# Kernel tuning notes

Hardware: AMD Instinct MI355X
Metric: run time of the kernel (lower is better)

The kernel has to match this reference:

```python
import jax, jax.numpy as jnp
import numpy as np

N, E = 50000, 800000
D_IN, HID, H, C, E_DIM = 128, 128, 4, 32, 32  # C = HID // H


def setup_inputs() -> dict:
    key = jax.random.key(0)
    ks = jax.random.split(key, 16)
    def lin(k, fan_in, fan_out):
        return jax.random.normal(k, (fan_in, fan_out), jnp.float32) / np.sqrt(fan_in)
    return {
        "x": jax.random.normal(ks[0], (N, D_IN), jnp.float32),
        "edge_index": jax.random.randint(ks[1], (2, E), 0, N, jnp.int32),
        "edge_attr": jax.random.normal(ks[2], (E, E_DIM), jnp.float32),
        # TransformerConv params (bias=True on q/k/v and skip; lin_edge has no bias in PyG)
        "Wq": lin(ks[3], D_IN, HID), "bq": jnp.zeros((HID,), jnp.float32),
        "Wk": lin(ks[4], D_IN, HID), "bk": jnp.zeros((HID,), jnp.float32),
        "Wv": lin(ks[5], D_IN, HID), "bv": jnp.zeros((HID,), jnp.float32),
        "We": lin(ks[6], E_DIM, HID),
        "Wskip": lin(ks[7], D_IN, HID), "bskip": jnp.zeros((HID,), jnp.float32),
        # MLP([HID, HID, HID]) -> two Linear layers, GELU(tanh) after each (plain_last=False)
        "W1": lin(ks[8], HID, HID), "b1": jnp.zeros((HID,), jnp.float32),
        "W2": lin(ks[9], HID, HID), "b2": jnp.zeros((HID,), jnp.float32),
    }


def reference(x, edge_index, edge_attr, Wq, bq, Wk, bk, Wv, bv, We, Wskip, bskip, W1, b1, W2, b2):
    src, dst = edge_index[0], edge_index[1]  # messages flow src(j) -> dst(i)
    n = x.shape[0]
    q = (x @ Wq + bq).reshape(n, H, C)
    k = (x @ Wk + bk).reshape(n, H, C)
    v = (x @ Wv + bv).reshape(n, H, C)
    e = (edge_attr @ We).reshape(-1, H, C)          # [E,H,C]
    kj = k[src] + e                                  # gather + edge lift
    vj = v[src] + e
    alpha = jnp.einsum("ehc,ehc->eh", q[dst], kj) / np.sqrt(C)  # [E,H]
    # segment softmax over destination neighborhoods (PyG softmax semantics)
    amax = jax.ops.segment_max(alpha, dst, num_segments=n)      # [N,H]
    amax = jnp.where(jnp.isfinite(amax), amax, 0.0)
    ex = jnp.exp(alpha - amax[dst])
    denom = jax.ops.segment_sum(ex, dst, num_segments=n)
    alpha = ex / (denom[dst] + 1e-16)
    # (attention dropout p=0.3 is inactive in eval mode)
    agg = jax.ops.segment_sum(vj * alpha[:, :, None], dst, num_segments=n)  # [N,H,C]
    out = agg.reshape(n, HID) + (x @ Wskip + bskip)  # concat heads + root skip
    # residual MLP: gelu(tanh) after every layer since plain_last=False, norm=None
    h = jax.nn.gelu(out @ W1 + b1, approximate=True)
    h = jax.nn.gelu(h @ W2 + b2, approximate=True)
    return out + h
```

## Files before the change

### kernel.cpp

```cpp
#include <hip/hip_runtime.h>
#include <math.h>


#define D 128
#define EDIM 32

using bf16x8 = __attribute__((ext_vector_type(8))) short;
using f32x4  = __attribute__((ext_vector_type(4))) float;
using ushort8 = __attribute__((ext_vector_type(8))) unsigned short;

__device__ inline unsigned short f2bf(float f) {
    unsigned int u = __float_as_uint(f);
    u += 0x7FFFu + ((u >> 16) & 1u);
    return (unsigned short)(u >> 16);
}
__device__ inline float bf2f(unsigned short h) {
    return __uint_as_float(((unsigned int)h) << 16);
}
__device__ inline float gelu_fast(float x) {
    float x3 = x * x * x;
    float u = 0.7978845608028654f * (x + 0.044715f * x3);
    float t = 1.f - 2.f / (__expf(2.f * u) + 1.f);
    return 0.5f * x * (1.f + t);
}
__device__ inline float quad_add(float x) {
    int a = __builtin_amdgcn_update_dpp(0, __float_as_int(x), 0xB1, 0xF, 0xF, true);
    x += __int_as_float(a);
    a = __builtin_amdgcn_update_dpp(0, __float_as_int(x), 0x4E, 0xF, 0xF, true);
    x += __int_as_float(a);
    return x;
}

__device__ inline bf16x8 ldsB(const unsigned short* sw, int col, int kk0) {
    return *(const bf16x8*)(sw + col * 128 + (kk0 ^ ((col & 7) << 3)));
}

__global__ __launch_bounds__(256) void prep_wt(
    const float* __restrict__ Wq, const float* __restrict__ Wk,
    const float* __restrict__ Wv, const float* __restrict__ Wsk,
    const float* __restrict__ W1, const float* __restrict__ W2,
    const float* __restrict__ We, const float* __restrict__ bq,
    unsigned short* __restrict__ Wt, float* __restrict__ bqE)
{
    int t = blockIdx.x * 256 + threadIdx.x;
    int m = t >> 14;
    int r = t & 16383;
    if (m >= 8) {
        if (r < 128) {
            const int hb = r & 96, k = r & 31;
            const float* wek = We + (size_t)k * D + hb;
            float s = 0.f;
#pragma unroll 8
            for (int c = 0; c < 32; ++c) s = fmaf(bq[hb + c], wek[c], s);
            bqE[r] = s;
        }
        return;
    }
    int col = r & 127, kk = r >> 7;
    float v;
    if (m < 6) {
        const float* W = (m == 0) ? Wq : (m == 1) ? Wk : (m == 2) ? Wv
                       : (m == 3) ? Wsk : (m == 4) ? W1 : W2;
        v = W[(size_t)kk * D + col];
    } else if (m == 6) {
        const int hb = col & 96;
        const float* wqr = Wq + (size_t)kk * D + hb;
        const float* wer = We + (size_t)(col & 31) * D + hb;
        float s = 0.f;
#pragma unroll 8
        for (int c = 0; c < 32; ++c) s = fmaf(wqr[c], wer[c], s);
        v = s;
    } else {
        v = ((kk >> 5) == (col >> 5)) ? We[(size_t)(kk & 31) * D + col] : 0.f;
    }
    Wt[(size_t)m * 16384 + (size_t)col * 128 + (kk ^ ((col & 7) << 3))] = f2bf(v);
}

__global__ __launch_bounds__(256) void gemm_qkvs(
    const float* __restrict__ x, const unsigned short* __restrict__ Wt,
    const float* __restrict__ bq, const float* __restrict__ bk,
    const float* __restrict__ bv, const float* __restrict__ bs,
    const float* __restrict__ bqE,
    unsigned short* __restrict__ QA, unsigned short* __restrict__ KV,
    float* __restrict__ S, int N)
{
    __shared__ unsigned short sw[16384];
    const int m = blockIdx.y;
    const int widx = (m < 4) ? m : 6;
    const int t = threadIdx.x;
    const int lane = t & 63;
    const int w = t >> 6;
    const int row0 = blockIdx.x * 64 + w * 16;
    const int lrow = lane & 15;
    const int kb = (lane >> 4) * 8;
    const int rq = (lane >> 4) * 4;

    const unsigned short* gsrc = Wt + (size_t)widx * 16384;
    ushort8 stg[8];
#pragma unroll
    for (int it = 0; it < 8; ++it)
        stg[it] = *(const ushort8*)(gsrc + (t + it * 256) * 8);

    bf16x8 af[4];
    {
        int ar = row0 + lrow; if (ar > N - 1) ar = N - 1;
        const float* xr = x + (size_t)ar * D + kb;
#pragma unroll
        for (int kf = 0; kf < 4; ++kf) {
            float4 p0 = *(const float4*)(xr + kf * 32);
            float4 p1 = *(const float4*)(xr + kf * 32 + 4);
            bf16x8 a;
            a[0] = (short)f2bf(p0.x); a[1] = (short)f2bf(p0.y);
            a[2] = (short)f2bf(p0.z); a[3] = (short)f2bf(p0.w);
            a[4] = (short)f2bf(p1.x); a[5] = (short)f2bf(p1.y);
            a[6] = (short)f2bf(p1.z); a[7] = (short)f2bf(p1.w);
            af[kf] = a;
        }
    }

#pragma unroll
    for (int it = 0; it < 8; ++it)
        *(ushort8*)(&sw[(t + it * 256) * 8]) = stg[it];
    __syncthreads();

    const float* bias = (m == 0) ? bq : (m == 1) ? bk : (m == 2) ? bv
                      : (m == 3) ? bs : bqE;
    f32x4 acc[8];
#pragma unroll
    for (int nf = 0; nf < 8; ++nf) acc[nf] = (f32x4){0.f, 0.f, 0.f, 0.f};
#pragma unroll
    for (int nf = 0; nf < 8; ++nf) {
        const int col = nf * 16 + lrow;
#pragma unroll
        for (int kf = 0; kf < 4; ++kf)
            acc[nf] = __builtin_amdgcn_mfma_f32_16x16x32_bf16(
                af[kf], ldsB(sw, col, kf * 32 + kb), acc[nf], 0, 0, 0);
    }
#pragma unroll
    for (int nf = 0; nf < 8; ++nf) {
        const int col = nf * 16 + lrow;
        const float bb = bias[col];
#pragma unroll
        for (int i = 0; i < 4; ++i) {
            int r = row0 + rq + i;
            if (r < N) {
                float v = acc[nf][i] + bb;
                if (m == 0)      QA[(size_t)r * 256 + col]       = f2bf(v);
                else if (m == 1) KV[(size_t)r * 256 + col]       = f2bf(v);
                else if (m == 2) KV[(size_t)r * 256 + 128 + col] = f2bf(v);
                else if (m == 3) S[(size_t)r * D + col]          = v;
                else             QA[(size_t)r * 256 + 128 + col] = f2bf(v);
            }
        }
    }
}

__global__ __launch_bounds__(256) void hist_kernel(
    const int* __restrict__ EI, int* __restrict__ deg, int E)
{
    int e = blockIdx.x * 256 + threadIdx.x;
    if (e < E) atomicAdd(&deg[EI[E + e]], 1);
}

__global__ __launch_bounds__(1024) void scanA(
    const int* __restrict__ deg, int* __restrict__ rowptr,
    int* __restrict__ psums, int N)
{
    __shared__ int tmp[1024];
    const int t = threadIdx.x;
    const int i = blockIdx.x * 1024 + t;
    int v = (i < N) ? deg[i] : 0;
    tmp[t] = v;
    __syncthreads();
    for (int off = 1; off < 1024; off <<= 1) {
        int add = (t >= off) ? tmp[t - off] : 0;
        __syncthreads();
        tmp[t] += add;
        __syncthreads();
    }
    if (i < N) rowptr[i + 1] = tmp[t];
    if (t == 1023) psums[blockIdx.x] = tmp[1023];
}

__global__ __launch_bounds__(1024) void scanB(int* __restrict__ psums, int nb)
{
    __shared__ int tmp[1024];
    const int t = threadIdx.x;
    int v = (t < nb) ? psums[t] : 0;
    tmp[t] = v;
    __syncthreads();
    for (int off = 1; off < 1024; off <<= 1) {
        int add = (t >= off) ? tmp[t - off] : 0;
        __syncthreads();
        tmp[t] += add;
        __syncthreads();
    }
    if (t < nb) psums[t] = tmp[t] - v;
}

__global__ __launch_bounds__(256) void scanC(
    int* __restrict__ rowptr, int* __restrict__ cursor,
    const int* __restrict__ psums, int N)
{
    int i = blockIdx.x * 256 + threadIdx.x;
    if (i == 0) { rowptr[0] = 0; cursor[0] = 0; }
    if (i < N) {
        int val = rowptr[i + 1] + psums[i >> 10];
        rowptr[i + 1] = val;
        if (i + 1 < N) cursor[i + 1] = val;
    }
}

__global__ __launch_bounds__(256) void scatter_kernel(
    const int* __restrict__ EI, const float* __restrict__ EA,
    int* __restrict__ cursor, int* __restrict__ srcs,
    unsigned short* __restrict__ EAP, int E)
{
    int e = blockIdx.x * 256 + threadIdx.x;
    if (e >= E) return;
    int dst = EI[E + e];
    int pos = atomicAdd(&cursor[dst], 1);
    srcs[pos] = EI[e];
    const float4* s4 = (const float4*)(EA + (size_t)e * EDIM);
    unsigned short* op = EAP + (size_t)pos * EDIM;
#pragma unroll
    for (int j = 0; j < 4; ++j) {
        float4 a = s4[2 * j], b = s4[2 * j + 1];
        ushort8 u;
        u[0] = f2bf(a.x); u[1] = f2bf(a.y); u[2] = f2bf(a.z); u[3] = f2bf(a.w);
        u[4] = f2bf(b.x); u[5] = f2bf(b.y); u[6] = f2bf(b.z); u[7] = f2bf(b.w);
        *(ushort8*)(op + j * 8) = u;
    }
}

__global__ __launch_bounds__(256) void gather_pass(
    const int* __restrict__ rowptr, const int* __restrict__ srcs,
    const unsigned short* __restrict__ EAP,
    const unsigned short* __restrict__ QA, const unsigned short* __restrict__ KV,
    float* __restrict__ SB, unsigned short* __restrict__ SAS, int N)
{
    const int lane = threadIdx.x & 63;
    const int wid = threadIdx.x >> 6;
    const int n = blockIdx.x * 4 + wid;
    if (n >= N) return;
    const int g = lane & 15;
    const int grp = lane >> 4;
    const int eoff = (g & 3) * 8;

    float q8[8], qe8[8];
    {
        const unsigned short* qa = QA + (size_t)n * 256 + g * 8;
        bf16x8 qb  = *(const bf16x8*)(qa);
        bf16x8 qeb = *(const bf16x8*)(qa + 128);
#pragma unroll
        for (int j = 0; j < 8; ++j) {
            q8[j]  = bf2f((unsigned short)qb[j]);
            qe8[j] = bf2f((unsigned short)qeb[j]);
        }
    }

    float acc[8], sa[8], den = 0.f;
#pragma unroll
    for (int j = 0; j < 8; ++j) { acc[j] = 0.f; sa[j] = 0.f; }

    const int i0 = rowptr[n], i1 = rowptr[n + 1];

    int iA = i0 + grp, iB = iA + 4;
    int sA = (iA < i1) ? srcs[iA] : -1;
    int sB = (iB < i1) ? srcs[iB] : -1;

    for (int b = i0; b < i1; b += 8) {
        const int iA2 = iA + 8, iB2 = iB + 8;
        const int sA2 = (iA2 < i1) ? srcs[iA2] : -1;
        const int sB2 = (iB2 < i1) ? srcs[iB2] : -1;

        bf16x8 kA = {0,0,0,0,0,0,0,0}, vA = kA, eA = kA;
        bf16x8 kB = kA, vB = kA, eB = kA;
        if (sA >= 0) {
            const unsigned short* kv = KV + (size_t)sA * 256 + g * 8;
            kA = *(const bf16x8*)(kv);
            vA = *(const bf16x8*)(kv + 128);
            eA = *(const bf16x8*)(EAP + (size_t)iA * EDIM + eoff);
        }
        if (sB >= 0) {
            const unsigned short* kv = KV + (size_t)sB * 256 + g * 8;
            kB = *(const bf16x8*)(kv);
            vB = *(const bf16x8*)(kv + 128);
            eB = *(const bf16x8*)(EAP + (size_t)iB * EDIM + eoff);
        }

        {
            float ef[8];
            float p = 0.f;
#pragma unroll
            for (int j = 0; j < 8; ++j) {
                ef[j] = bf2f((unsigned short)eA[j]);
                p = fmaf(q8[j], bf2f((unsigned short)kA[j]),
                         fmaf(ef[j], qe8[j], p));
            }
            p = quad_add(p);
            const float ex = (sA >= 0) ? __expf(p * 0.17677669529663689f) : 0.f;
            den += ex;
#pragma unroll
            for (int j = 0; j < 8; ++j) {
                acc[j] = fmaf(ex, bf2f((unsigned short)vA[j]), acc[j]);
                sa[j]  = fmaf(ex, ef[j], sa[j]);
            }
        }
        {
            float ef[8];
            float p = 0.f;
#pragma unroll
            for (int j = 0; j < 8; ++j) {
                ef[j] = bf2f((unsigned short)eB[j]);
                p = fmaf(q8[j], bf2f((unsigned short)kB[j]),
                         fmaf(ef[j], qe8[j], p));
            }
            p = quad_add(p);
            const float ex = (sB >= 0) ? __expf(p * 0.17677669529663689f) : 0.f;
            den += ex;
#pragma unroll
            for (int j = 0; j < 8; ++j) {
                acc[j] = fmaf(ex, bf2f((unsigned short)vB[j]), acc[j]);
                sa[j]  = fmaf(ex, ef[j], sa[j]);
            }
        }
        iA = iA2; iB = iB2; sA = sA2; sB = sB2;
    }

#pragma unroll
    for (int off = 16; off <= 32; off <<= 1) {
        den += __shfl_xor(den, off, 64);
#pragma unroll
        for (int j = 0; j < 8; ++j) {
            acc[j] += __shfl_xor(acc[j], off, 64);
            sa[j]  += __shfl_xor(sa[j],  off, 64);
        }
    }

    if (grp == 0) {
        const float rden = 1.f / (den + 1e-16f);
        float* so = SB + (size_t)n * D + g * 8;
        unsigned short* po = SAS + (size_t)n * D + g * 8;
#pragma unroll
        for (int j = 0; j < 8; ++j) {
            so[j] = fmaf(acc[j], rden, so[j]);
            po[j] = f2bf(sa[j] * rden);
        }
    }
}

__global__ __launch_bounds__(256) void combine_mlp1(
    float* __restrict__ SB, const unsigned short* __restrict__ SAS,
    const unsigned short* __restrict__ WtC, const unsigned short* __restrict__ Wt1,
    const float* __restrict__ b1, unsigned short* __restrict__ H1, int N)
{
    __shared__ unsigned short sw[16384];
    __shared__ unsigned short bounce[64 * 136];
    const int t = threadIdx.x;
    const int lane = t & 63;
    const int w = t >> 6;
    const int row0 = blockIdx.x * 64 + w * 16;
    const int lrow = lane & 15;
    const int kb = (lane >> 4) * 8;
    const int rq = (lane >> 4) * 4;

    ushort8 stg[8];
#pragma unroll
    for (int it = 0; it < 8; ++it)
        stg[it] = *(const ushort8*)(WtC + (t + it * 256) * 8);

    bf16x8 af[4];
    {
        int ar = row0 + lrow; if (ar > N - 1) ar = N - 1;
        const unsigned short* xr = SAS + (size_t)ar * D + kb;
#pragma unroll
        for (int kf = 0; kf < 4; ++kf) af[kf] = *(const bf16x8*)(xr + kf * 32);
    }
    f32x4 acc[8];
#pragma unroll
    for (int nf = 0; nf < 8; ++nf) {
        const int col = nf * 16 + lrow;
#pragma unroll
        for (int i = 0; i < 4; ++i) {
            int r = row0 + rq + i;
            acc[nf][i] = (r < N) ? SB[(size_t)r * D + col] : 0.f;
        }
    }

#pragma unroll
    for (int it = 0; it < 8; ++it)
        *(ushort8*)(&sw[(t + it * 256) * 8]) = stg[it];
    __syncthreads();

#pragma unroll
    for (int nf = 0; nf < 8; ++nf) {
        const int col = nf * 16 + lrow;
#pragma unroll
        for (int kf = 0; kf < 4; ++kf)
            acc[nf] = __builtin_amdgcn_mfma_f32_16x16x32_bf16(
                af[kf], ldsB(sw, col, kf * 32 + kb), acc[nf], 0, 0, 0);
    }
    __syncthreads();

#pragma unroll
    for (int it = 0; it < 8; ++it)
        stg[it] = *(const ushort8*)(Wt1 + (t + it * 256) * 8);
#pragma unroll
    for (int nf = 0; nf < 8; ++nf) {
        const int col = nf * 16 + lrow;
#pragma unroll
        for (int i = 0; i < 4; ++i) {
            int r = row0 + rq + i;
            float v = acc[nf][i];
            bounce[(w * 16 + rq + i) * 136 + col] = f2bf(v);
            if (r < N) SB[(size_t)r * D + col] = v;
        }
    }
#pragma unroll
    for (int it = 0; it < 8; ++it)
        *(ushort8*)(&sw[(t + it * 256) * 8]) = stg[it];
    __syncthreads();

    bf16x8 af2[4];
#pragma unroll
    for (int kf = 0; kf < 4; ++kf)
        af2[kf] = *(const bf16x8*)(&bounce[(w * 16 + lrow) * 136 + kb + kf * 32]);
    f32x4 acc2[8];
#pragma unroll
    for (int nf = 0; nf < 8; ++nf) acc2[nf] = (f32x4){0.f, 0.f, 0.f, 0.f};
#pragma unroll
    for (int nf = 0; nf < 8; ++nf) {
        const int col = nf * 16 + lrow;
#pragma unroll
        for (int kf = 0; kf < 4; ++kf)
            acc2[nf] = __builtin_amdgcn_mfma_f32_16x16x32_bf16(
                af2[kf], ldsB(sw, col, kf * 32 + kb), acc2[nf], 0, 0, 0);
    }
#pragma unroll
    for (int nf = 0; nf < 8; ++nf) {
        const int col = nf * 16 + lrow;
        const float bb = b1[col];
#pragma unroll
        for (int i = 0; i < 4; ++i) {
            int r = row0 + rq + i;
            if (r < N) H1[(size_t)r * D + col] = f2bf(gelu_fast(acc2[nf][i] + bb));
        }
    }
}

__global__ __launch_bounds__(256) void mlp2_kernel(
    const unsigned short* __restrict__ H1, const float* __restrict__ OUT,
    const unsigned short* __restrict__ Wt2, const float* __restrict__ b2,
    float* __restrict__ FINAL, int N)
{
    __shared__ unsigned short sw[16384];
    const int t = threadIdx.x;
    const int lane = t & 63;
    const int w = t >> 6;
    const int row0 = blockIdx.x * 64 + w * 16;
    const int lrow = lane & 15;
    const int kb = (lane >> 4) * 8;
    const int rq = (lane >> 4) * 4;

    ushort8 stg[8];
#pragma unroll
    for (int it = 0; it < 8; ++it)
        stg[it] = *(const ushort8*)(Wt2 + (t + it * 256) * 8);

    bf16x8 af[4];
    {
        int ar = row0 + lrow; if (ar > N - 1) ar = N - 1;
        const unsigned short* xr = H1 + (size_t)ar * D + kb;
#pragma unroll
        for (int kf = 0; kf < 4; ++kf) af[kf] = *(const bf16x8*)(xr + kf * 32);
    }

#pragma unroll
    for (int it = 0; it < 8; ++it)
        *(ushort8*)(&sw[(t + it * 256) * 8]) = stg[it];
    __syncthreads();

    f32x4 acc[8];
#pragma unroll
    for (int nf = 0; nf < 8; ++nf) acc[nf] = (f32x4){0.f, 0.f, 0.f, 0.f};
#pragma unroll
    for (int nf = 0; nf < 8; ++nf) {
        const int col = nf * 16 + lrow;
#pragma unroll
        for (int kf = 0; kf < 4; ++kf)
            acc[nf] = __builtin_amdgcn_mfma_f32_16x16x32_bf16(
                af[kf], ldsB(sw, col, kf * 32 + kb), acc[nf], 0, 0, 0);
    }
#pragma unroll
    for (int nf = 0; nf < 8; ++nf) {
        const int col = nf * 16 + lrow;
        const float bb = b2[col];
#pragma unroll
        for (int i = 0; i < 4; ++i) {
            int r = row0 + rq + i;
            if (r < N) {
                size_t o = (size_t)r * D + col;
                FINAL[o] = OUT[o] + gelu_fast(acc[nf][i] + bb);
            }
        }
    }
}

extern "C" void kernel_launch(void* const* d_in, const int* in_sizes, int n_in,
                              void* d_out, int out_size, void* d_ws, size_t ws_size,
                              hipStream_t stream)
{
    const float* x   = (const float*)d_in[0];
    const int*   EI  = (const int*)  d_in[1];
    const float* EA  = (const float*)d_in[2];
    const float* Wq  = (const float*)d_in[3];
    const float* bq  = (const float*)d_in[4];
    const float* Wk  = (const float*)d_in[5];
    const float* bk  = (const float*)d_in[6];
    const float* Wv  = (const float*)d_in[7];
    const float* bv  = (const float*)d_in[8];
    const float* We  = (const float*)d_in[9];
    const float* Wsk = (const float*)d_in[10];
    const float* bsk = (const float*)d_in[11];
    const float* W1  = (const float*)d_in[12];
    const float* b1  = (const float*)d_in[13];
    const float* W2  = (const float*)d_in[14];
    const float* b2  = (const float*)d_in[15];

    const int N = in_sizes[0] / D;
    const int E = in_sizes[1] / 2;

    char* p = (char*)d_ws;
    auto alloc = [&](size_t bytes) -> void* {
        void* r = (void*)p;
        p += (bytes + 255) & ~(size_t)255;
        return r;
    };
    float*          Sb     = (float*)         alloc((size_t)N * D * 4);
    unsigned short* QAb    = (unsigned short*)alloc((size_t)N * 256 * 2);
    unsigned short* KVb    = (unsigned short*)alloc((size_t)N * 256 * 2);
    unsigned short* SASb   = (unsigned short*)alloc((size_t)N * D * 2);
    unsigned short* EAPb   = (unsigned short*)alloc((size_t)E * EDIM * 2);
    int*            srcsb  = (int*)           alloc((size_t)E * 4);
    unsigned short* Wt     = (unsigned short*)alloc((size_t)8 * 16384 * 2);
    float*          bqEb   = (float*)         alloc((size_t)128 * 4);
    int*            deg    = (int*)           alloc((size_t)N * 4);
    int*            rowptr = (int*)           alloc((size_t)(N + 1) * 4);
    int*            cursor = (int*)           alloc((size_t)(N + 1) * 4);
    int*            psums  = (int*)           alloc((size_t)1024 * 4);

    unsigned short* H1b = QAb;

    hipMemsetAsync(deg, 0, (size_t)N * sizeof(int), stream);

    const int NB = (N + 63) / 64;
    const int EB = (E + 255) / 256;
    const int SB_ = (N + 1023) / 1024;

    prep_wt<<<513, 256, 0, stream>>>(Wq, Wk, Wv, Wsk, W1, W2, We, bq, Wt, bqEb);

    gemm_qkvs<<<dim3(NB, 5), 256, 0, stream>>>(x, Wt, bq, bk, bv, bsk, bqEb,
                                               QAb, KVb, Sb, N);

    hist_kernel<<<EB, 256, 0, stream>>>(EI, deg, E);
    scanA<<<SB_, 1024, 0, stream>>>(deg, rowptr, psums, N);
    scanB<<<1, 1024, 0, stream>>>(psums, SB_);
    scanC<<<(N + 255) / 256, 256, 0, stream>>>(rowptr, cursor, psums, N);
    scatter_kernel<<<EB, 256, 0, stream>>>(EI, EA, cursor, srcsb, EAPb, E);

    gather_pass<<<(N + 3) / 4, 256, 0, stream>>>(
        rowptr, srcsb, EAPb, QAb, KVb, Sb, SASb, N);

    combine_mlp1<<<NB, 256, 0, stream>>>(Sb, SASb, Wt + (size_t)7 * 16384,
                                         Wt + (size_t)4 * 16384, b1, H1b, N);
    mlp2_kernel<<<NB, 256, 0, stream>>>(H1b, Sb, Wt + (size_t)5 * 16384, b2,
                                        (float*)d_out, N);
}
```

Before: 299.2 us.

## Merge prep with histogram, scatter with QKV GEMM, and fuse both MLP layers

The weight-prep kernel now also runs the degree histogram in extra blocks, and the CSR scatter runs in the same launch as the QKV/skip GEMM through a flat block index. The two MLP kernels become one: the combined output stays in registers, and the first MLP activation goes through LDS instead of a global H1 buffer. This removes several launches, the H1 write and read, and the re-read of the output in the second MLP. In exchange, the fused MLP kernel uses more registers and LDS, and the mixed-role launches give heterogeneous blocks that may balance poorly.

```diff
diff --git a/kernel.cpp b/kernel.cpp
--- a/kernel.cpp
+++ b/kernel.cpp
@@ -35,13 +35,19 @@
     return *(const bf16x8*)(sw + col * 128 + (kk0 ^ ((col & 7) << 3)));
 }
 
-__global__ __launch_bounds__(256) void prep_wt(
+__global__ __launch_bounds__(256) void prep_wt_hist(
     const float* __restrict__ Wq, const float* __restrict__ Wk,
     const float* __restrict__ Wv, const float* __restrict__ Wsk,
     const float* __restrict__ W1, const float* __restrict__ W2,
     const float* __restrict__ We, const float* __restrict__ bq,
-    unsigned short* __restrict__ Wt, float* __restrict__ bqE)
-{
+    unsigned short* __restrict__ Wt, float* __restrict__ bqE,
+    const int* __restrict__ EI, int* __restrict__ deg, int E)
+{
+    if (blockIdx.x >= 513) {
+        int e = (blockIdx.x - 513) * 256 + threadIdx.x;
+        if (e < E) atomicAdd(&deg[EI[E + e]], 1);
+        return;
+    }
     int t = blockIdx.x * 256 + threadIdx.x;
     int m = t >> 14;
     int r = t & 16383;
@@ -76,21 +82,95 @@
     Wt[(size_t)m * 16384 + (size_t)col * 128 + (kk ^ ((col & 7) << 3))] = f2bf(v);
 }
 
-__global__ __launch_bounds__(256) void gemm_qkvs(
+__global__ __launch_bounds__(1024) void scanA(
+    const int* __restrict__ deg, int* __restrict__ rowptr,
+    int* __restrict__ psums, int N)
+{
+    __shared__ int tmp[1024];
+    const int t = threadIdx.x;
+    const int i = blockIdx.x * 1024 + t;
+    int v = (i < N) ? deg[i] : 0;
+    tmp[t] = v;
+    __syncthreads();
+    for (int off = 1; off < 1024; off <<= 1) {
+        int add = (t >= off) ? tmp[t - off] : 0;
+        __syncthreads();
+        tmp[t] += add;
+        __syncthreads();
+    }
+    if (i < N) rowptr[i + 1] = tmp[t];
+    if (t == 1023) psums[blockIdx.x] = tmp[1023];
+}
+
+__global__ __launch_bounds__(1024) void scanB(int* __restrict__ psums, int nb)
+{
+    __shared__ int tmp[1024];
+    const int t = threadIdx.x;
+    int v = (t < nb) ? psums[t] : 0;
+    tmp[t] = v;
+    __syncthreads();
+    for (int off = 1; off < 1024; off <<= 1) {
+        int add = (t >= off) ? tmp[t - off] : 0;
+        __syncthreads();
+        tmp[t] += add;
+        __syncthreads();
+    }
+    if (t < nb) psums[t] = tmp[t] - v;
+}
+
+__global__ __launch_bounds__(256) void scanC(
+    int* __restrict__ rowptr, int* __restrict__ cursor,
+    const int* __restrict__ psums, int N)
+{
+    int i = blockIdx.x * 256 + threadIdx.x;
+    if (i == 0) { rowptr[0] = 0; cursor[0] = 0; }
+    if (i < N) {
+        int val = rowptr[i + 1] + psums[i >> 10];
+        rowptr[i + 1] = val;
+        if (i + 1 < N) cursor[i + 1] = val;
+    }
+}
+
+__global__ __launch_bounds__(256) void mega_scatter_gemm(
+    const int* __restrict__ EI, const float* __restrict__ EA,
+    int* __restrict__ cursor, int* __restrict__ srcs,
+    unsigned short* __restrict__ EAP, int E, int EB,
     const float* __restrict__ x, const unsigned short* __restrict__ Wt,
     const float* __restrict__ bq, const float* __restrict__ bk,
     const float* __restrict__ bv, const float* __restrict__ bs,
     const float* __restrict__ bqE,
     unsigned short* __restrict__ QA, unsigned short* __restrict__ KV,
-    float* __restrict__ S, int N)
+    float* __restrict__ S, int N, int NB)
 {
     __shared__ unsigned short sw[16384];
-    const int m = blockIdx.y;
+    const int t = threadIdx.x;
+
+    if ((int)blockIdx.x < EB) {
+        int e = blockIdx.x * 256 + t;
+        if (e >= E) return;
+        int dst = EI[E + e];
+        int pos = atomicAdd(&cursor[dst], 1);
+        srcs[pos] = EI[e];
+        const float4* s4 = (const float4*)(EA + (size_t)e * EDIM);
+        unsigned short* op = EAP + (size_t)pos * EDIM;
+#pragma unroll
+        for (int j = 0; j < 4; ++j) {
+            float4 a = s4[2 * j], b = s4[2 * j + 1];
+            ushort8 u;
+            u[0] = f2bf(a.x); u[1] = f2bf(a.y); u[2] = f2bf(a.z); u[3] = f2bf(a.w);
+            u[4] = f2bf(b.x); u[5] = f2bf(b.y); u[6] = f2bf(b.z); u[7] = f2bf(b.w);
+            *(ushort8*)(op + j * 8) = u;
+        }
+        return;
+    }
+
+    const int bid = blockIdx.x - EB;
+    const int m = bid / NB;
+    const int bx = bid - m * NB;
     const int widx = (m < 4) ? m : 6;
-    const int t = threadIdx.x;
     const int lane = t & 63;
     const int w = t >> 6;
-    const int row0 = blockIdx.x * 64 + w * 16;
+    const int row0 = bx * 64 + w * 16;
     const int lrow = lane & 15;
     const int kb = (lane >> 4) * 8;
     const int rq = (lane >> 4) * 4;
@@ -155,84 +235,6 @@
     }
 }
 
-__global__ __launch_bounds__(256) void hist_kernel(
-    const int* __restrict__ EI, int* __restrict__ deg, int E)
-{
-    int e = blockIdx.x * 256 + threadIdx.x;
-    if (e < E) atomicAdd(&deg[EI[E + e]], 1);
-}
-
-__global__ __launch_bounds__(1024) void scanA(
-    const int* __restrict__ deg, int* __restrict__ rowptr,
-    int* __restrict__ psums, int N)
-{
-    __shared__ int tmp[1024];
-    const int t = threadIdx.x;
-    const int i = blockIdx.x * 1024 + t;
-    int v = (i < N) ? deg[i] : 0;
-    tmp[t] = v;
-    __syncthreads();
-    for (int off = 1; off < 1024; off <<= 1) {
-        int add = (t >= off) ? tmp[t - off] : 0;
-        __syncthreads();
-        tmp[t] += add;
-        __syncthreads();
-    }
-    if (i < N) rowptr[i + 1] = tmp[t];
-    if (t == 1023) psums[blockIdx.x] = tmp[1023];
-}
-
-__global__ __launch_bounds__(1024) void scanB(int* __restrict__ psums, int nb)
-{
-    __shared__ int tmp[1024];
-    const int t = threadIdx.x;
-    int v = (t < nb) ? psums[t] : 0;
-    tmp[t] = v;
-    __syncthreads();
-    for (int off = 1; off < 1024; off <<= 1) {
-        int add = (t >= off) ? tmp[t - off] : 0;
-        __syncthreads();
-        tmp[t] += add;
-        __syncthreads();
-    }
-    if (t < nb) psums[t] = tmp[t] - v;
-}
-
-__global__ __launch_bounds__(256) void scanC(
-    int* __restrict__ rowptr, int* __restrict__ cursor,
-    const int* __restrict__ psums, int N)
-{
-    int i = blockIdx.x * 256 + threadIdx.x;
-    if (i == 0) { rowptr[0] = 0; cursor[0] = 0; }
-    if (i < N) {
-        int val = rowptr[i + 1] + psums[i >> 10];
-        rowptr[i + 1] = val;
-        if (i + 1 < N) cursor[i + 1] = val;
-    }
-}
-
-__global__ __launch_bounds__(256) void scatter_kernel(
-    const int* __restrict__ EI, const float* __restrict__ EA,
-    int* __restrict__ cursor, int* __restrict__ srcs,
-    unsigned short* __restrict__ EAP, int E)
-{
-    int e = blockIdx.x * 256 + threadIdx.x;
-    if (e >= E) return;
-    int dst = EI[E + e];
-    int pos = atomicAdd(&cursor[dst], 1);
-    srcs[pos] = EI[e];
-    const float4* s4 = (const float4*)(EA + (size_t)e * EDIM);
-    unsigned short* op = EAP + (size_t)pos * EDIM;
-#pragma unroll
-    for (int j = 0; j < 4; ++j) {
-        float4 a = s4[2 * j], b = s4[2 * j + 1];
-        ushort8 u;
-        u[0] = f2bf(a.x); u[1] = f2bf(a.y); u[2] = f2bf(a.z); u[3] = f2bf(a.w);
-        u[4] = f2bf(b.x); u[5] = f2bf(b.y); u[6] = f2bf(b.z); u[7] = f2bf(b.w);
-        *(ushort8*)(op + j * 8) = u;
-    }
-}
-
 __global__ __launch_bounds__(256) void gather_pass(
     const int* __restrict__ rowptr, const int* __restrict__ srcs,
     const unsigned short* __restrict__ EAP,
@@ -350,10 +352,12 @@
     }
 }
 
-__global__ __launch_bounds__(256) void combine_mlp1(
-    float* __restrict__ SB, const unsigned short* __restrict__ SAS,
+__global__ __launch_bounds__(256) void fused_mlp(
+    const float* __restrict__ SB, const unsigned short* __restrict__ SAS,
     const unsigned short* __restrict__ WtC, const unsigned short* __restrict__ Wt1,
-    const float* __restrict__ b1, unsigned short* __restrict__ H1, int N)
+    const unsigned short* __restrict__ Wt2,
+    const float* __restrict__ b1, const float* __restrict__ b2,
+    float* __restrict__ FINAL, int N)
 {
     __shared__ unsigned short sw[16384];
     __shared__ unsigned short bounce[64 * 136];
@@ -377,17 +381,16 @@
 #pragma unroll
         for (int kf = 0; kf < 4; ++kf) af[kf] = *(const bf16x8*)(xr + kf * 32);
     }
-    f32x4 acc[8];
+    f32x4 out[8];
 #pragma unroll
     for (int nf = 0; nf < 8; ++nf) {
         const int col = nf * 16 + lrow;
 #pragma unroll
         for (int i = 0; i < 4; ++i) {
             int r = row0 + rq + i;
-            acc[nf][i] = (r < N) ? SB[(size_t)r * D + col] : 0.f;
-        }
-    }
-
+            out[nf][i] = (r < N) ? SB[(size_t)r * D + col] : 0.f;
+        }
+    }
 #pragma unroll
     for (int it = 0; it < 8; ++it)
         *(ushort8*)(&sw[(t + it * 256) * 8]) = stg[it];
@@ -398,8 +401,8 @@
         const int col = nf * 16 + lrow;
 #pragma unroll
         for (int kf = 0; kf < 4; ++kf)
-            acc[nf] = __builtin_amdgcn_mfma_f32_16x16x32_bf16(
-                af[kf], ldsB(sw, col, kf * 32 + kb), acc[nf], 0, 0, 0);
+            out[nf] = __builtin_amdgcn_mfma_f32_16x16x32_bf16(
+                af[kf], ldsB(sw, col, kf * 32 + kb), out[nf], 0, 0, 0);
     }
     __syncthreads();
 
@@ -410,12 +413,8 @@
     for (int nf = 0; nf < 8; ++nf) {
         const int col = nf * 16 + lrow;
 #pragma unroll
-        for (int i = 0; i < 4; ++i) {
-            int r = row0 + rq + i;
-            float v = acc[nf][i];
-            bounce[(w * 16 + rq + i) * 136 + col] = f2bf(v);
-            if (r < N) SB[(size_t)r * D + col] = v;
-        }
+        for (int i = 0; i < 4; ++i)
+            bounce[(w * 16 + rq + i) * 136 + col] = f2bf(out[nf][i]);
     }
 #pragma unroll
     for (int it = 0; it < 8; ++it)
@@ -437,72 +436,48 @@
             acc2[nf] = __builtin_amdgcn_mfma_f32_16x16x32_bf16(
                 af2[kf], ldsB(sw, col, kf * 32 + kb), acc2[nf], 0, 0, 0);
     }
+    __syncthreads();
+
+#pragma unroll
+    for (int it = 0; it < 8; ++it)
+        stg[it] = *(const ushort8*)(Wt2 + (t + it * 256) * 8);
 #pragma unroll
     for (int nf = 0; nf < 8; ++nf) {
         const int col = nf * 16 + lrow;
         const float bb = b1[col];
+#pragma unroll
+        for (int i = 0; i < 4; ++i)
+            bounce[(w * 16 + rq + i) * 136 + col] = f2bf(gelu_fast(acc2[nf][i] + bb));
+    }
+#pragma unroll
+    for (int it = 0; it < 8; ++it)
+        *(ushort8*)(&sw[(t + it * 256) * 8]) = stg[it];
+    __syncthreads();
+
+    bf16x8 af3[4];
+#pragma unroll
+    for (int kf = 0; kf < 4; ++kf)
+        af3[kf] = *(const bf16x8*)(&bounce[(w * 16 + lrow) * 136 + kb + kf * 32]);
+    f32x4 acc3[8];
+#pragma unroll
+    for (int nf = 0; nf < 8; ++nf) acc3[nf] = (f32x4){0.f, 0.f, 0.f, 0.f};
+#pragma unroll
+    for (int nf = 0; nf < 8; ++nf) {
+        const int col = nf * 16 + lrow;
+#pragma unroll
+        for (int kf = 0; kf < 4; ++kf)
+            acc3[nf] = __builtin_amdgcn_mfma_f32_16x16x32_bf16(
+                af3[kf], ldsB(sw, col, kf * 32 + kb), acc3[nf], 0, 0, 0);
+    }
+#pragma unroll
+    for (int nf = 0; nf < 8; ++nf) {
+        const int col = nf * 16 + lrow;
+        const float bb = b2[col];
 #pragma unroll
         for (int i = 0; i < 4; ++i) {
             int r = row0 + rq + i;
-            if (r < N) H1[(size_t)r * D + col] = f2bf(gelu_fast(acc2[nf][i] + bb));
-        }
-    }
-}
-
-__global__ __launch_bounds__(256) void mlp2_kernel(
-    const unsigned short* __restrict__ H1, const float* __restrict__ OUT,
-    const unsigned short* __restrict__ Wt2, const float* __restrict__ b2,
-    float* __restrict__ FINAL, int N)
-{
-    __shared__ unsigned short sw[16384];
-    const int t = threadIdx.x;
-    const int lane = t & 63;
-    const int w = t >> 6;
-    const int row0 = blockIdx.x * 64 + w * 16;
-    const int lrow = lane & 15;
-    const int kb = (lane >> 4) * 8;
-    const int rq = (lane >> 4) * 4;
-
-    ushort8 stg[8];
-#pragma unroll
-    for (int it = 0; it < 8; ++it)
-        stg[it] = *(const ushort8*)(Wt2 + (t + it * 256) * 8);
-
-    bf16x8 af[4];
-    {
-        int ar = row0 + lrow; if (ar > N - 1) ar = N - 1;
-        const unsigned short* xr = H1 + (size_t)ar * D + kb;
-#pragma unroll
-        for (int kf = 0; kf < 4; ++kf) af[kf] = *(const bf16x8*)(xr + kf * 32);
-    }
-
-#pragma unroll
-    for (int it = 0; it < 8; ++it)
-        *(ushort8*)(&sw[(t + it * 256) * 8]) = stg[it];
-    __syncthreads();
-
-    f32x4 acc[8];
-#pragma unroll
-    for (int nf = 0; nf < 8; ++nf) acc[nf] = (f32x4){0.f, 0.f, 0.f, 0.f};
-#pragma unroll
-    for (int nf = 0; nf < 8; ++nf) {
-        const int col = nf * 16 + lrow;
-#pragma unroll
-        for (int kf = 0; kf < 4; ++kf)
-            acc[nf] = __builtin_amdgcn_mfma_f32_16x16x32_bf16(
-                af[kf], ldsB(sw, col, kf * 32 + kb), acc[nf], 0, 0, 0);
-    }
-#pragma unroll
-    for (int nf = 0; nf < 8; ++nf) {
-        const int col = nf * 16 + lrow;
-        const float bb = b2[col];
-#pragma unroll
-        for (int i = 0; i < 4; ++i) {
-            int r = row0 + rq + i;
-            if (r < N) {
-                size_t o = (size_t)r * D + col;
-                FINAL[o] = OUT[o] + gelu_fast(acc[nf][i] + bb);
-            }
+            if (r < N)
+                FINAL[(size_t)r * D + col] = out[nf][i] + gelu_fast(acc3[nf][i] + bb);
         }
     }
 }
@@ -550,30 +525,29 @@
     int*            cursor = (int*)           alloc((size_t)(N + 1) * 4);
     int*            psums  = (int*)           alloc((size_t)1024 * 4);
 
-    unsigned short* H1b = QAb;
-
     hipMemsetAsync(deg, 0, (size_t)N * sizeof(int), stream);
 
     const int NB = (N + 63) / 64;
     const int EB = (E + 255) / 256;
     const int SB_ = (N + 1023) / 1024;
 
-    prep_wt<<<513, 256, 0, stream>>>(Wq, Wk, Wv, Wsk, W1, W2, We, bq, Wt, bqEb);
-
-    gemm_qkvs<<<dim3(NB, 5), 256, 0, stream>>>(x, Wt, bq, bk, bv, bsk, bqEb,
-                                               QAb, KVb, Sb, N);
-
-    hist_kernel<<<EB, 256, 0, stream>>>(EI, deg, E);
+    prep_wt_hist<<<513 + EB, 256, 0, stream>>>(Wq, Wk, Wv, Wsk, W1, W2, We, bq,
+                                               Wt, bqEb, EI, deg, E);
+
     scanA<<<SB_, 1024, 0, stream>>>(deg, rowptr, psums, N);
     scanB<<<1, 1024, 0, stream>>>(psums, SB_);
     scanC<<<(N + 255) / 256, 256, 0, stream>>>(rowptr, cursor, psums, N);
-    scatter_kernel<<<EB, 256, 0, stream>>>(EI, EA, cursor, srcsb, EAPb, E);
+
+    mega_scatter_gemm<<<EB + 5 * NB, 256, 0, stream>>>(
+        EI, EA, cursor, srcsb, EAPb, E, EB,
+        x, Wt, bq, bk, bv, bsk, bqEb, QAb, KVb, Sb, N, NB);
 
     gather_pass<<<(N + 3) / 4, 256, 0, stream>>>(
         rowptr, srcsb, EAPb, QAb, KVb, Sb, SASb, N);
 
-    combine_mlp1<<<NB, 256, 0, stream>>>(Sb, SASb, Wt + (size_t)7 * 16384,
-                                         Wt + (size_t)4 * 16384, b1, H1b, N);
-    mlp2_kernel<<<NB, 256, 0, stream>>>(H1b, Sb, Wt + (size_t)5 * 16384, b2,
-                                        (float*)d_out, N);
-}
+    fused_mlp<<<NB, 256, 0, stream>>>(Sb, SASb,
+                                      Wt + (size_t)7 * 16384,
+                                      Wt + (size_t)4 * 16384,
+                                      Wt + (size_t)5 * 16384,
+                                      b1, b2, (float*)d_out, N);
+}
```

Result: faster. 270.3 us (-9.7%).
